# Optimization experiments

Hardware: AMD Instinct MI355X
Metric: run time of the kernel (lower is better)

The kernel has to match this reference:

```python
import jax, jax.numpy as jnp
import numpy as np

N = 50000          # nodes
E = 800000         # edges (before self loops)
IN_C = 128
HEADS = 4
D = 64             # out_per_head
HID = HEADS * D    # 256
OUT_C = 128
NEG_SLOPE = 0.2


def setup_inputs() -> dict:
    key = jax.random.key(0)
    ks = jax.random.split(key, 20)
    x = jax.random.normal(ks[0], (N, IN_C), dtype=jnp.float32)
    edge_index = jax.random.randint(ks[1], (2, E), 0, N, dtype=jnp.int32)
    s = 0.05
    params = {}
    dims = [IN_C, HID, HID]
    for i in range(3):
        params[f"W{i+1}"] = jax.random.normal(ks[2 + 4 * i], (dims[i], HID), dtype=jnp.float32) * s
        params[f"a_src{i+1}"] = jax.random.normal(ks[3 + 4 * i], (HEADS, D), dtype=jnp.float32) * s
        params[f"a_dst{i+1}"] = jax.random.normal(ks[4 + 4 * i], (HEADS, D), dtype=jnp.float32) * s
        params[f"b{i+1}"] = jnp.zeros((HID,), dtype=jnp.float32)
    params["head_W"] = jax.random.normal(ks[14], (HID, OUT_C), dtype=jnp.float32) * s
    params["head_b"] = jnp.zeros((OUT_C,), dtype=jnp.float32)
    return {"x": x, "edge_index": edge_index, **params}


def _gat_layer(x, src, dst, W, a_src, a_dst, b):
    # project: [N, heads, D]
    h = (x @ W).reshape(-1, HEADS, D)
    # per-node attention halves: [N, heads]
    alpha_s = jnp.einsum("nhd,hd->nh", h, a_src)
    alpha_d = jnp.einsum("nhd,hd->nh", h, a_dst)
    # per-edge logits: [E, heads]
    logits = jax.nn.leaky_relu(alpha_s[src] + alpha_d[dst], negative_slope=NEG_SLOPE)
    # segment softmax over incoming edges of each dst node
    seg_max = jax.ops.segment_max(logits, dst, num_segments=N)
    e = jnp.exp(logits - seg_max[dst])
    seg_sum = jax.ops.segment_sum(e, dst, num_segments=N)
    alpha = e / (seg_sum[dst] + 1e-16)
    # weighted messages, scatter-aggregate: [N, heads, D]
    msg = h[src] * alpha[:, :, None]
    out = jax.ops.segment_sum(msg, dst, num_segments=N)
    return out.reshape(-1, HID) + b


def reference(x, edge_index, W1, a_src1, a_dst1, b1, W2, a_src2, a_dst2, b2,
              W3, a_src3, a_dst3, b3, head_W, head_b):
    # add self loops once (add_self_loops=True in every GATConv)
    loop = jnp.arange(N, dtype=edge_index.dtype)
    src = jnp.concatenate([edge_index[0], loop])
    dst = jnp.concatenate([edge_index[1], loop])
    h = x
    layers = [(W1, a_src1, a_dst1, b1), (W2, a_src2, a_dst2, b2), (W3, a_src3, a_dst3, b3)]
    for (W, a_s, a_d, b) in layers:
        h = jax.nn.elu(_gat_layer(h, src, dst, W, a_s, a_d, b))
        # dropout inactive in eval mode
    graph_emb = jnp.mean(h, axis=0)          # global_mean_pool over single graph
    logits = graph_emb @ head_W + head_b     # [OUT_C]
    return logits
```

## Files before the change

kernel.cpp:

```cpp
#include <hip/hip_runtime.h>
#include <stdint.h>

#define NN 50000
#define EE 800000
#define ET 850000
#define INC 128
#define HID 256
#define OUTC 128
#define NB ((NN + 255) / 256)
#define GDEG ((ET + 255) / 256)
#define GTRP 640

typedef __attribute__((ext_vector_type(4))) float f32x4;
typedef __attribute__((ext_vector_type(8))) short s16x8;
typedef __attribute__((ext_vector_type(4))) short s16x4;

static __device__ __forceinline__ float b2f(unsigned short u){
  union { float f; unsigned int i; } v; v.i = ((unsigned int)u) << 16; return v.f;
}
static __device__ __forceinline__ unsigned short f2b(float f){
  union { float f; unsigned int i; } v; v.f = f;
  unsigned int r = v.i + 0x7FFFu + ((v.i >> 16) & 1u);
  return (unsigned short)(r >> 16);
}

__global__ void k_init(const int* __restrict__ ei, int* __restrict__ cnt,
                       const float* __restrict__ W1, const float* __restrict__ W2,
                       const float* __restrict__ W3, unsigned short* __restrict__ T1,
                       unsigned short* __restrict__ T2, unsigned short* __restrict__ T3,
                       float* __restrict__ pool){
  int b = blockIdx.x, tid = threadIdx.x;
  if (b < GDEG){
    int e = b * 256 + tid;
    if (e < ET){
      int d = (e < EE) ? ei[EE + e] : (e - EE);
      atomicAdd(&cnt[d], 1);
    }
  } else if (b < GDEG + GTRP){
    int bb = b - GDEG;
    const float* W; unsigned short* WT; int K, base;
    if (bb < 128)      { W = W1; WT = T1; K = 128; base = 0; }
    else if (bb < 384) { W = W2; WT = T2; K = 256; base = 128; }
    else               { W = W3; WT = T3; K = 256; base = 384; }
    int idx = (bb - base) * 256 + tid;
    int k = idx >> 8, c = idx & 255;
    WT[c * K + k] = f2b(W[idx]);
  } else {
    pool[tid] = 0.f;
  }
}

__global__ void k_blockscan(int* __restrict__ cnt, int* __restrict__ off,
                            int* __restrict__ bsum){
  __shared__ int s[256];
  int b = blockIdx.x, tid = threadIdx.x;
  int i = b * 256 + tid;
  int v = (i < NN) ? cnt[i] : 0;
  if (i < NN) cnt[i] = 0;
  s[tid] = v; __syncthreads();
  #pragma unroll
  for (int o = 1; o < 256; o <<= 1){
    int t = (tid >= o) ? s[tid - o] : 0; __syncthreads();
    s[tid] += t; __syncthreads();
  }
  if (i < NN) off[i] = s[tid] - v;
  if (tid == 255) bsum[b] = s[255];
}

__global__ void k_scanb(const int* __restrict__ bsum, int* __restrict__ bbase){
  __shared__ int s[256];
  int tid = threadIdx.x;
  int v = (tid < NB) ? bsum[tid] : 0;
  s[tid] = v; __syncthreads();
  #pragma unroll
  for (int o = 1; o < 256; o <<= 1){
    int t = (tid >= o) ? s[tid - o] : 0; __syncthreads();
    s[tid] += t; __syncthreads();
  }
  if (tid < NB) bbase[tid] = s[tid] - v;
}

__global__ void k_scatter(const int* __restrict__ ei, const int* __restrict__ off,
                          const int* __restrict__ bbase, int* __restrict__ cnt,
                          int* __restrict__ ssrc){
  int e = blockIdx.x * 256 + threadIdx.x;
  if (e >= ET) return;
  int s, d;
  if (e < EE){ s = ei[e]; d = ei[EE + e]; } else { s = e - EE; d = s; }
  int p = off[d] + bbase[d >> 8] + atomicAdd(&cnt[d], 1);
  ssrc[p] = s;
}

template<bool AF32>
__global__ __launch_bounds__(256) void k_gemm_fused(const void* __restrict__ Av,
    const unsigned short* __restrict__ WT,
    const float* __restrict__ a_src, const float* __restrict__ a_dst,
    unsigned short* __restrict__ C, float* __restrict__ as_, float* __restrict__ ad_,
    int M, int K){
  __shared__ unsigned short sA[2][32][72];
  int tid = threadIdx.x;
  int wave = tid >> 6, lane = tid & 63;
  int bm0 = blockIdx.x * 32;
  int wc0 = wave * 64;
  f32x4 acc[2][4];
  #pragma unroll
  for (int i = 0; i < 2; i++)
    #pragma unroll
    for (int j = 0; j < 4; j++) acc[i][j] = (f32x4){0.f, 0.f, 0.f, 0.f};

  s16x8 rg;
  int r0 = tid >> 3, kb0 = (tid & 7) * 8;

  auto ldA = [&](int k0){
    int gr = bm0 + r0;
    if constexpr (AF32){
      const float* A = (const float*)Av;
      unsigned short t[8] = {0,0,0,0,0,0,0,0};
      if (gr < M){
        const float4* p = (const float4*)(A + (size_t)gr * K + k0 + kb0);
        float4 v0 = p[0], v1 = p[1];
        t[0]=f2b(v0.x); t[1]=f2b(v0.y); t[2]=f2b(v0.z); t[3]=f2b(v0.w);
        t[4]=f2b(v1.x); t[5]=f2b(v1.y); t[6]=f2b(v1.z); t[7]=f2b(v1.w);
      }
      rg = *(s16x8*)t;
    } else {
      const unsigned short* A = (const unsigned short*)Av;
      s16x8 v = (s16x8){0,0,0,0,0,0,0,0};
      if (gr < M) v = *(const s16x8*)(A + (size_t)gr * K + k0 + kb0);
      rg = v;
    }
  };

  int T = K >> 6;
  ldA(0); *(s16x8*)&sA[0][r0][kb0] = rg;
  __syncthreads();
  for (int t = 0; t < T; t++){
    int k0 = t << 6;
    if (t + 1 < T) ldA(k0 + 64);
    int cur = t & 1;
    s16x8 af[2][2], bf[2][4];
    #pragma unroll
    for (int half = 0; half < 2; half++){
      int kl = half * 32 + (lane >> 4) * 8;
      af[half][0] = *(const s16x8*)&sA[cur][lane & 15][kl];
      af[half][1] = *(const s16x8*)&sA[cur][16 + (lane & 15)][kl];
      #pragma unroll
      for (int ni = 0; ni < 4; ni++)
        bf[half][ni] = *(const s16x8*)(WT + (size_t)(wc0 + ni * 16 + (lane & 15)) * K + k0 + kl);
    }
    #pragma unroll
    for (int half = 0; half < 2; half++)
      #pragma unroll
      for (int mi = 0; mi < 2; mi++)
        #pragma unroll
        for (int ni = 0; ni < 4; ni++)
          acc[mi][ni] = __builtin_amdgcn_mfma_f32_16x16x32_bf16(af[half][mi], bf[half][ni], acc[mi][ni], 0, 0, 0);
    if (t + 1 < T) *(s16x8*)&sA[cur ^ 1][r0][kb0] = rg;
    __syncthreads();
  }

  #pragma unroll
  for (int mi = 0; mi < 2; mi++){
    #pragma unroll
    for (int ni = 0; ni < 4; ni++){
      int col = wc0 + ni * 16 + (lane & 15);
      int rb = mi * 16 + (lane >> 4) * 4;
      #pragma unroll
      for (int r = 0; r < 4; r++){
        int row = rb + r;
        if (bm0 + row < M) C[(size_t)(bm0 + row) * HID + col] = f2b(acc[mi][ni][r]);
      }
    }
  }
  float asv[4], adv[4];
  #pragma unroll
  for (int ni = 0; ni < 4; ni++){
    int d = wc0 + ni * 16 + (lane & 15);
    asv[ni] = a_src[d];
    adv[ni] = a_dst[d];
  }
  #pragma unroll
  for (int mi = 0; mi < 2; mi++){
    #pragma unroll
    for (int r = 0; r < 4; r++){
      float ps = 0.f, pd = 0.f;
      #pragma unroll
      for (int ni = 0; ni < 4; ni++){
        float cv = acc[mi][ni][r];
        ps += cv * asv[ni];
        pd += cv * adv[ni];
      }
      #pragma unroll
      for (int m = 1; m < 16; m <<= 1){
        ps += __shfl_xor(ps, m, 64);
        pd += __shfl_xor(pd, m, 64);
      }
      int row = bm0 + mi * 16 + (lane >> 4) * 4 + r;
      if ((lane & 15) == 0 && row < M){
        as_[(size_t)row * 4 + wave] = ps;
        ad_[(size_t)row * 4 + wave] = pd;
      }
    }
  }
}

__global__ __launch_bounds__(256) void k_aggregate(const int* __restrict__ off,
    const int* __restrict__ bbase, const int* __restrict__ ssrc,
    const float* __restrict__ as_, const float* __restrict__ ad_,
    const unsigned short* __restrict__ h, const float* __restrict__ bias,
    unsigned short* __restrict__ out){
  int gid = blockIdx.x * 256 + threadIdx.x;
  int wid = gid >> 6, lane = gid & 63;
  if (wid >= NN) return;
  int start = off[wid] + bbase[wid >> 8];
  int end = (wid + 1 < NN) ? (off[wid + 1] + bbase[(wid + 1) >> 8]) : ET;
  int e1 = end - 1;
  int hq = lane >> 4;
  float ad2 = ad_[(size_t)wid * 4 + hq];
  float sA_ = 0.f, sB_ = 0.f;
  f32x4 A = {0,0,0,0}, B = {0,0,0,0}, Cc = {0,0,0,0}, D = {0,0,0,0};

  int p = start;
  int j0 = ssrc[p];
  int j1 = ssrc[min(p + 1, e1)], j2 = ssrc[min(p + 2, e1)], j3 = ssrc[min(p + 3, e1)];
  int j4 = ssrc[min(p + 4, e1)], j5 = ssrc[min(p + 5, e1)];
  int j6 = ssrc[min(p + 6, e1)], j7 = ssrc[min(p + 7, e1)];
  s16x4 r0 = *(const s16x4*)(h + (size_t)j0 * HID + lane * 4);
  s16x4 r1 = *(const s16x4*)(h + (size_t)j1 * HID + lane * 4);
  s16x4 r2 = *(const s16x4*)(h + (size_t)j2 * HID + lane * 4);
  s16x4 r3 = *(const s16x4*)(h + (size_t)j3 * HID + lane * 4);
  float a0 = as_[(size_t)j0 * 4 + hq], a1 = as_[(size_t)j1 * 4 + hq];
  float a2 = as_[(size_t)j2 * 4 + hq], a3 = as_[(size_t)j3 * 4 + hq];

  for (; p + 11 < end; p += 4){
    s16x4 u0 = *(const s16x4*)(h + (size_t)j4 * HID + lane * 4);
    s16x4 u1 = *(const s16x4*)(h + (size_t)j5 * HID + lane * 4);
    s16x4 u2 = *(const s16x4*)(h + (size_t)j6 * HID + lane * 4);
    s16x4 u3 = *(const s16x4*)(h + (size_t)j7 * HID + lane * 4);
    float b0 = as_[(size_t)j4 * 4 + hq], b1 = as_[(size_t)j5 * 4 + hq];
    float b2 = as_[(size_t)j6 * 4 + hq], b3 = as_[(size_t)j7 * 4 + hq];
    int t0 = ssrc[p + 8], t1 = ssrc[p + 9], t2 = ssrc[p + 10], t3 = ssrc[p + 11];
    float l0 = a0 + ad2; l0 = fmaxf(l0, 0.2f * l0);
    float l1 = a1 + ad2; l1 = fmaxf(l1, 0.2f * l1);
    float l2 = a2 + ad2; l2 = fmaxf(l2, 0.2f * l2);
    float l3 = a3 + ad2; l3 = fmaxf(l3, 0.2f * l3);
    float w0 = __expf(l0), w1 = __expf(l1), w2 = __expf(l2), w3 = __expf(l3);
    sA_ += w0 + w2; sB_ += w1 + w3;
    #pragma unroll
    for (int c = 0; c < 4; c++){
      A[c]  += w0 * b2f((unsigned short)r0[c]);
      B[c]  += w1 * b2f((unsigned short)r1[c]);
      Cc[c] += w2 * b2f((unsigned short)r2[c]);
      D[c]  += w3 * b2f((unsigned short)r3[c]);
    }
    j0 = j4; j1 = j5; j2 = j6; j3 = j7;
    j4 = t0; j5 = t1; j6 = t2; j7 = t3;
    r0 = u0; r1 = u1; r2 = u2; r3 = u3;
    a0 = b0; a1 = b1; a2 = b2; a3 = b3;
  }
  for (; p + 3 < end; p += 4){
    s16x4 u0 = *(const s16x4*)(h + (size_t)j4 * HID + lane * 4);
    s16x4 u1 = *(const s16x4*)(h + (size_t)j5 * HID + lane * 4);
    s16x4 u2 = *(const s16x4*)(h + (size_t)j6 * HID + lane * 4);
    s16x4 u3 = *(const s16x4*)(h + (size_t)j7 * HID + lane * 4);
    float b0 = as_[(size_t)j4 * 4 + hq], b1 = as_[(size_t)j5 * 4 + hq];
    float b2 = as_[(size_t)j6 * 4 + hq], b3 = as_[(size_t)j7 * 4 + hq];
    int t0 = ssrc[min(p + 8, e1)],  t1 = ssrc[min(p + 9, e1)];
    int t2 = ssrc[min(p + 10, e1)], t3 = ssrc[min(p + 11, e1)];
    float l0 = a0 + ad2; l0 = fmaxf(l0, 0.2f * l0);
    float l1 = a1 + ad2; l1 = fmaxf(l1, 0.2f * l1);
    float l2 = a2 + ad2; l2 = fmaxf(l2, 0.2f * l2);
    float l3 = a3 + ad2; l3 = fmaxf(l3, 0.2f * l3);
    float w0 = __expf(l0), w1 = __expf(l1), w2 = __expf(l2), w3 = __expf(l3);
    sA_ += w0 + w2; sB_ += w1 + w3;
    #pragma unroll
    for (int c = 0; c < 4; c++){
      A[c]  += w0 * b2f((unsigned short)r0[c]);
      B[c]  += w1 * b2f((unsigned short)r1[c]);
      Cc[c] += w2 * b2f((unsigned short)r2[c]);
      D[c]  += w3 * b2f((unsigned short)r3[c]);
    }
    j0 = j4; j1 = j5; j2 = j6; j3 = j7;
    j4 = t0; j5 = t1; j6 = t2; j7 = t3;
    r0 = u0; r1 = u1; r2 = u2; r3 = u3;
    a0 = b0; a1 = b1; a2 = b2; a3 = b3;
  }
  int rem = end - p;
  if (rem > 0){
    float l = a0 + ad2; l = fmaxf(l, 0.2f * l);
    float w = __expf(l); sA_ += w;
    #pragma unroll
    for (int c = 0; c < 4; c++) A[c]  += w * b2f((unsigned short)r0[c]);
  }
  if (rem > 1){
    float l = a1 + ad2; l = fmaxf(l, 0.2f * l);
    float w = __expf(l); sB_ += w;
    #pragma unroll
    for (int c = 0; c < 4; c++) B[c]  += w * b2f((unsigned short)r1[c]);
  }
  if (rem > 2){
    float l = a2 + ad2; l = fmaxf(l, 0.2f * l);
    float w = __expf(l); sA_ += w;
    #pragma unroll
    for (int c = 0; c < 4; c++) Cc[c] += w * b2f((unsigned short)r2[c]);
  }

  float inv = 1.f / (sA_ + sB_ + 1e-16f);
  float4 bv = *(const float4*)(bias + lane * 4);
  float o0 = (A[0] + B[0] + Cc[0] + D[0]) * inv + bv.x;
  float o1 = (A[1] + B[1] + Cc[1] + D[1]) * inv + bv.y;
  float o2 = (A[2] + B[2] + Cc[2] + D[2]) * inv + bv.z;
  float o3 = (A[3] + B[3] + Cc[3] + D[3]) * inv + bv.w;
  o0 = o0 > 0.f ? o0 : (__expf(o0) - 1.f);
  o1 = o1 > 0.f ? o1 : (__expf(o1) - 1.f);
  o2 = o2 > 0.f ? o2 : (__expf(o2) - 1.f);
  o3 = o3 > 0.f ? o3 : (__expf(o3) - 1.f);
  s16x4 ov;
  ov[0] = (short)f2b(o0); ov[1] = (short)f2b(o1);
  ov[2] = (short)f2b(o2); ov[3] = (short)f2b(o3);
  *(s16x4*)(out + (size_t)wid * HID + lane * 4) = ov;
}

__global__ __launch_bounds__(256) void k_pool(const unsigned short* __restrict__ X,
                                              float* __restrict__ pool){
  int b = blockIdx.x, c = threadIdx.x;
  int n0 = b * 64, n1 = min(n0 + 64, NN);
  float acc = 0.f;
  for (int n = n0; n < n1; n++) acc += b2f(X[(size_t)n * HID + c]);
  atomicAdd(&pool[c], acc);
}

__global__ void k_head(const float* __restrict__ pool, const float* __restrict__ hW,
                       const float* __restrict__ hb, float* __restrict__ outp){
  int o = threadIdx.x;
  float acc = hb[o];
  const float invN = 1.f / (float)NN;
  for (int c = 0; c < HID; c++) acc += pool[c] * invN * hW[c * OUTC + o];
  outp[o] = acc;
}

extern "C" void kernel_launch(void* const* d_in, const int* in_sizes, int n_in,
                              void* d_out, int out_size, void* d_ws, size_t ws_size,
                              hipStream_t stream){
  const float* x  = (const float*)d_in[0];
  const int* ei   = (const int*)d_in[1];
  const float* W[3]   = {(const float*)d_in[2],  (const float*)d_in[6],  (const float*)d_in[10]};
  const float* Asr[3] = {(const float*)d_in[3],  (const float*)d_in[7],  (const float*)d_in[11]};
  const float* Adt[3] = {(const float*)d_in[4],  (const float*)d_in[8],  (const float*)d_in[12]};
  const float* B[3]   = {(const float*)d_in[5],  (const float*)d_in[9],  (const float*)d_in[13]};
  const float* hW = (const float*)d_in[14];
  const float* hb = (const float*)d_in[15];

  char* w = (char*)d_ws; size_t o = 0;
  auto alloc = [&](size_t b) -> void* { void* p = w + o; o = (o + b + 255) & ~(size_t)255; return p; };
  int* cnt  = (int*)alloc((size_t)NN * 4);
  int* off  = (int*)alloc((size_t)NN * 4);
  int* ssrc = (int*)alloc((size_t)ET * 4);
  int* bsum = (int*)alloc((size_t)NB * 4);
  int* bbase= (int*)alloc((size_t)NB * 4);
  unsigned short* hbuf = (unsigned short*)alloc((size_t)NN * HID * 2);
  float* as_ = (float*)alloc((size_t)NN * 4 * 4);
  float* ad_ = (float*)alloc((size_t)NN * 4 * 4);
  unsigned short* X0 = (unsigned short*)alloc((size_t)NN * HID * 2);
  unsigned short* X1 = (unsigned short*)alloc((size_t)NN * HID * 2);
  unsigned short* WT1 = (unsigned short*)alloc((size_t)INC * HID * 2);
  unsigned short* WT2 = (unsigned short*)alloc((size_t)HID * HID * 2);
  unsigned short* WT3 = (unsigned short*)alloc((size_t)HID * HID * 2);
  float* pool = (float*)alloc(256 * 4);

  hipMemsetAsync(cnt, 0, (size_t)NN * 4, stream);
  k_init<<<GDEG + GTRP + 1, 256, 0, stream>>>(ei, cnt, W[0], W[1], W[2], WT1, WT2, WT3, pool);
  k_blockscan<<<NB, 256, 0, stream>>>(cnt, off, bsum);
  k_scanb<<<1, 256, 0, stream>>>(bsum, bbase);
  k_scatter<<<GDEG, 256, 0, stream>>>(ei, off, bbase, cnt, ssrc);

  const unsigned short* WTs[3] = {WT1, WT2, WT3};
  unsigned short* outbuf[3] = {X0, X1, X0};
  int Ks[3] = {INC, HID, HID};
  const void* Ain = (const void*)x;
  int gB = (NN + 63) / 64;
  int gG = (NN + 31) / 32;
  int gW = (NN * 64 + 255) / 256;
  for (int l = 0; l < 3; l++){
    if (l == 0) k_gemm_fused<true ><<<gG, 256, 0, stream>>>(Ain, WTs[l], Asr[l], Adt[l], hbuf, as_, ad_, NN, Ks[l]);
    else        k_gemm_fused<false><<<gG, 256, 0, stream>>>(Ain, WTs[l], Asr[l], Adt[l], hbuf, as_, ad_, NN, Ks[l]);
    k_aggregate<<<gW, 256, 0, stream>>>(off, bbase, ssrc, as_, ad_, hbuf, B[l], outbuf[l]);
    Ain = (const void*)outbuf[l];
  }
  k_pool<<<gB, 256, 0, stream>>>(X0, pool);
  k_head<<<1, 128, 0, stream>>>(pool, hW, hb, (float*)d_out);
}
```

Measured before the change: 425.8 us.

## Cooperatively compute edge weights across lanes and batch 16 row gathers per wave

Restructures the per-node aggregation so each wave loads 16 edge source indices at once, with one lane per (edge, head) pair computing the attention weight. The indices and weights are then broadcast with shuffles, and up to 16 feature rows are gathered in one batch. This replaces the old scheme, where every lane redundantly loaded indices and attention scalars in a 4-wide software pipeline. It should raise memory-level parallelism and cut redundant scalar loads, at the cost of more shuffles, more registers and wasted lanes for low-degree nodes.

```diff
diff --git a/kernel.cpp b/kernel.cpp
--- a/kernel.cpp
+++ b/kernel.cpp
@@ -216,101 +216,43 @@
   int end = (wid + 1 < NN) ? (off[wid + 1] + bbase[(wid + 1) >> 8]) : ET;
   int e1 = end - 1;
   int hq = lane >> 4;
-  float ad2 = ad_[(size_t)wid * 4 + hq];
-  float sA_ = 0.f, sB_ = 0.f;
-  f32x4 A = {0,0,0,0}, B = {0,0,0,0}, Cc = {0,0,0,0}, D = {0,0,0,0};
-
-  int p = start;
-  int j0 = ssrc[p];
-  int j1 = ssrc[min(p + 1, e1)], j2 = ssrc[min(p + 2, e1)], j3 = ssrc[min(p + 3, e1)];
-  int j4 = ssrc[min(p + 4, e1)], j5 = ssrc[min(p + 5, e1)];
-  int j6 = ssrc[min(p + 6, e1)], j7 = ssrc[min(p + 7, e1)];
-  s16x4 r0 = *(const s16x4*)(h + (size_t)j0 * HID + lane * 4);
-  s16x4 r1 = *(const s16x4*)(h + (size_t)j1 * HID + lane * 4);
-  s16x4 r2 = *(const s16x4*)(h + (size_t)j2 * HID + lane * 4);
-  s16x4 r3 = *(const s16x4*)(h + (size_t)j3 * HID + lane * 4);
-  float a0 = as_[(size_t)j0 * 4 + hq], a1 = as_[(size_t)j1 * 4 + hq];
-  float a2 = as_[(size_t)j2 * 4 + hq], a3 = as_[(size_t)j3 * 4 + hq];
-
-  for (; p + 11 < end; p += 4){
-    s16x4 u0 = *(const s16x4*)(h + (size_t)j4 * HID + lane * 4);
-    s16x4 u1 = *(const s16x4*)(h + (size_t)j5 * HID + lane * 4);
-    s16x4 u2 = *(const s16x4*)(h + (size_t)j6 * HID + lane * 4);
-    s16x4 u3 = *(const s16x4*)(h + (size_t)j7 * HID + lane * 4);
-    float b0 = as_[(size_t)j4 * 4 + hq], b1 = as_[(size_t)j5 * 4 + hq];
-    float b2 = as_[(size_t)j6 * 4 + hq], b3 = as_[(size_t)j7 * 4 + hq];
-    int t0 = ssrc[p + 8], t1 = ssrc[p + 9], t2 = ssrc[p + 10], t3 = ssrc[p + 11];
-    float l0 = a0 + ad2; l0 = fmaxf(l0, 0.2f * l0);
-    float l1 = a1 + ad2; l1 = fmaxf(l1, 0.2f * l1);
-    float l2 = a2 + ad2; l2 = fmaxf(l2, 0.2f * l2);
-    float l3 = a3 + ad2; l3 = fmaxf(l3, 0.2f * l3);
-    float w0 = __expf(l0), w1 = __expf(l1), w2 = __expf(l2), w3 = __expf(l3);
-    sA_ += w0 + w2; sB_ += w1 + w3;
-    #pragma unroll
-    for (int c = 0; c < 4; c++){
-      A[c]  += w0 * b2f((unsigned short)r0[c]);
-      B[c]  += w1 * b2f((unsigned short)r1[c]);
-      Cc[c] += w2 * b2f((unsigned short)r2[c]);
-      D[c]  += w3 * b2f((unsigned short)r3[c]);
-    }
-    j0 = j4; j1 = j5; j2 = j6; j3 = j7;
-    j4 = t0; j5 = t1; j6 = t2; j7 = t3;
-    r0 = u0; r1 = u1; r2 = u2; r3 = u3;
-    a0 = b0; a1 = b1; a2 = b2; a3 = b3;
-  }
-  for (; p + 3 < end; p += 4){
-    s16x4 u0 = *(const s16x4*)(h + (size_t)j4 * HID + lane * 4);
-    s16x4 u1 = *(const s16x4*)(h + (size_t)j5 * HID + lane * 4);
-    s16x4 u2 = *(const s16x4*)(h + (size_t)j6 * HID + lane * 4);
-    s16x4 u3 = *(const s16x4*)(h + (size_t)j7 * HID + lane * 4);
-    float b0 = as_[(size_t)j4 * 4 + hq], b1 = as_[(size_t)j5 * 4 + hq];
-    float b2 = as_[(size_t)j6 * 4 + hq], b3 = as_[(size_t)j7 * 4 + hq];
-    int t0 = ssrc[min(p + 8, e1)],  t1 = ssrc[min(p + 9, e1)];
-    int t2 = ssrc[min(p + 10, e1)], t3 = ssrc[min(p + 11, e1)];
-    float l0 = a0 + ad2; l0 = fmaxf(l0, 0.2f * l0);
-    float l1 = a1 + ad2; l1 = fmaxf(l1, 0.2f * l1);
-    float l2 = a2 + ad2; l2 = fmaxf(l2, 0.2f * l2);
-    float l3 = a3 + ad2; l3 = fmaxf(l3, 0.2f * l3);
-    float w0 = __expf(l0), w1 = __expf(l1), w2 = __expf(l2), w3 = __expf(l3);
-    sA_ += w0 + w2; sB_ += w1 + w3;
-    #pragma unroll
-    for (int c = 0; c < 4; c++){
-      A[c]  += w0 * b2f((unsigned short)r0[c]);
-      B[c]  += w1 * b2f((unsigned short)r1[c]);
-      Cc[c] += w2 * b2f((unsigned short)r2[c]);
-      D[c]  += w3 * b2f((unsigned short)r3[c]);
-    }
-    j0 = j4; j1 = j5; j2 = j6; j3 = j7;
-    j4 = t0; j5 = t1; j6 = t2; j7 = t3;
-    r0 = u0; r1 = u1; r2 = u2; r3 = u3;
-    a0 = b0; a1 = b1; a2 = b2; a3 = b3;
-  }
-  int rem = end - p;
-  if (rem > 0){
-    float l = a0 + ad2; l = fmaxf(l, 0.2f * l);
-    float w = __expf(l); sA_ += w;
-    #pragma unroll
-    for (int c = 0; c < 4; c++) A[c]  += w * b2f((unsigned short)r0[c]);
-  }
-  if (rem > 1){
-    float l = a1 + ad2; l = fmaxf(l, 0.2f * l);
-    float w = __expf(l); sB_ += w;
-    #pragma unroll
-    for (int c = 0; c < 4; c++) B[c]  += w * b2f((unsigned short)r1[c]);
-  }
-  if (rem > 2){
-    float l = a2 + ad2; l = fmaxf(l, 0.2f * l);
-    float w = __expf(l); sA_ += w;
-    #pragma unroll
-    for (int c = 0; c < 4; c++) Cc[c] += w * b2f((unsigned short)r2[c]);
-  }
-
-  float inv = 1.f / (sA_ + sB_ + 1e-16f);
+  int hh = lane & 3;
+  int el = lane >> 2;
+  float ad_hh = ad_[(size_t)wid * 4 + hh];
+  float ssum = 0.f;
+  f32x4 acc = {0.f, 0.f, 0.f, 0.f};
+
+  for (int base = start; base < end; base += 16){
+    int nv = end - base; if (nv > 16) nv = 16;
+    int sidx = ssrc[min(base + el, e1)];
+    float lg = as_[(size_t)sidx * 4 + hh] + ad_hh;
+    lg = fmaxf(lg, 0.2f * lg);
+    float w = (el < nv) ? __expf(lg) : 0.f;
+    int idxs[16];
+    #pragma unroll
+    for (int j = 0; j < 16; j++) idxs[j] = __shfl(sidx, j * 4, 64);
+    s16x4 rows[16];
+    #pragma unroll
+    for (int j = 0; j < 16; j++){
+      if (j < nv) rows[j] = *(const s16x4*)(h + (size_t)idxs[j] * HID + lane * 4);
+    }
+    #pragma unroll
+    for (int j = 0; j < 16; j++){
+      if (j < nv){
+        float wj = __shfl(w, j * 4 + hq, 64);
+        ssum += wj;
+        #pragma unroll
+        for (int c = 0; c < 4; c++) acc[c] += wj * b2f((unsigned short)rows[j][c]);
+      }
+    }
+  }
+
+  float inv = 1.f / (ssum + 1e-16f);
   float4 bv = *(const float4*)(bias + lane * 4);
-  float o0 = (A[0] + B[0] + Cc[0] + D[0]) * inv + bv.x;
-  float o1 = (A[1] + B[1] + Cc[1] + D[1]) * inv + bv.y;
-  float o2 = (A[2] + B[2] + Cc[2] + D[2]) * inv + bv.z;
-  float o3 = (A[3] + B[3] + Cc[3] + D[3]) * inv + bv.w;
+  float o0 = acc[0] * inv + bv.x;
+  float o1 = acc[1] * inv + bv.y;
+  float o2 = acc[2] * inv + bv.z;
+  float o3 = acc[3] * inv + bv.w;
   o0 = o0 > 0.f ? o0 : (__expf(o0) - 1.f);
   o1 = o1 > 0.f ? o1 : (__expf(o1) - 1.f);
   o2 = o2 > 0.f ? o2 : (__expf(o2) - 1.f);
```

Result: slower. 441.1 us (+3.6%).
